# Kernel tuning notes

Hardware: AMD Instinct MI355X
Metric: run time of the kernel (lower is better)

The kernel has to match this reference:

```python
import jax, jax.numpy as jnp
import numpy as np

DIM = 512
NL = 4
P = 8
B = 4
L = 8192  # byte-level sequence length
LP = L // P  # patch-level sequence length


def _ln(x, g, b, eps=1e-5):
    m = jnp.mean(x, axis=-1, keepdims=True)
    v = jnp.mean((x - m) ** 2, axis=-1, keepdims=True)
    return (x - m) * jax.lax.rsqrt(v + eps) * g + b


def setup_inputs() -> dict:
    key = jax.random.key(0)
    ks = jax.random.split(key, 24)
    s = 0.02
    inp = {
        "bytes_in": jax.random.randint(ks[0], (B, L), 0, 256, dtype=jnp.int32),
        "byte_emb": jax.random.normal(ks[1], (256, DIM), jnp.float32) * s,
        # patch encoder Conv1d(kernel=stride=P): weight laid out [P, D_in, D_out]
        "enc_w": jax.random.normal(ks[2], (P, DIM, DIM), jnp.float32) * s,
        "enc_b": jnp.zeros((DIM,), jnp.float32),
        "hash_proj": jax.random.normal(ks[3], (DIM, DIM), jnp.float32) * s,
        # per-layer stacked params
        "qkv_w": jax.random.normal(ks[4], (NL, DIM, 3 * DIM), jnp.float32) * s,
        "qkv_b": jnp.zeros((NL, 3 * DIM), jnp.float32),
        "gate_w": jax.random.normal(ks[5], (NL, DIM, DIM), jnp.float32) * s,
        "gate_b": jnp.zeros((NL, DIM), jnp.float32),
        "ln1_g": jnp.ones((NL, DIM), jnp.float32),
        "ln1_b": jnp.zeros((NL, DIM), jnp.float32),
        "mlp_w1": jax.random.normal(ks[6], (NL, DIM, 4 * DIM), jnp.float32) * s,
        "mlp_b1": jnp.zeros((NL, 4 * DIM), jnp.float32),
        "mlp_w2": jax.random.normal(ks[7], (NL, 4 * DIM, DIM), jnp.float32) * s,
        "mlp_b2": jnp.zeros((NL, DIM), jnp.float32),
        "ln2_g": jnp.ones((NL, DIM), jnp.float32),
        "ln2_b": jnp.zeros((NL, DIM), jnp.float32),
        # patch decoder ConvTranspose1d(kernel=stride=P): weight [D_in, P, D_out]
        "dec_w": jax.random.normal(ks[8], (DIM, P, DIM), jnp.float32) * s,
        "dec_b": jnp.zeros((DIM,), jnp.float32),
        "head_w": jax.random.normal(ks[9], (DIM, 256), jnp.float32) * s,
        "head_b": jnp.zeros((256,), jnp.float32),
    }
    return inp


def reference(bytes_in, byte_emb, enc_w, enc_b, hash_proj,
              qkv_w, qkv_b, gate_w, gate_b, ln1_g, ln1_b,
              mlp_w1, mlp_b1, mlp_w2, mlp_b2, ln2_g, ln2_b,
              dec_w, dec_b, head_w, head_b):
    # byte embedding: [B, L, D]
    x = byte_emb[bytes_in]
    # non-overlapping Conv1d(kernel=stride=P) == patch-wise contraction
    xp = x.reshape(B, LP, P, DIM)
    x = jnp.einsum('blpd,pdo->blo', xp, enc_w) + enc_b  # [B, LP, D]
    # hash projection
    x = x + jnp.tanh(x @ hash_proj)
    for i in range(NL):
        # LinearLatentKernel
        h = _ln(x, ln1_g[i], ln1_b[i])
        qkv = h @ qkv_w[i] + qkv_b[i]
        q, k, v = jnp.split(qkv, 3, axis=-1)
        kv_state = jnp.cumsum(k * v, axis=1)
        g = jax.nn.sigmoid(h @ gate_w[i] + gate_b[i])
        x = x + q * kv_state * g
        # MLP
        h = _ln(x, ln2_g[i], ln2_b[i])
        h = jax.nn.gelu(h @ mlp_w1[i] + mlp_b1[i], approximate=False)
        x = x + h @ mlp_w2[i] + mlp_b2[i]
    # ConvTranspose1d(kernel=stride=P): each patch expands to P positions
    y = jnp.einsum('bld,dpo->blpo', x, dec_w).reshape(B, L, DIM) + dec_b
    logits = y @ head_w + head_b  # [B, L, 256]
    return logits
```

## Files before the change

kernel.cpp:

```cpp
#include <hip/hip_runtime.h>
#include <hip/hip_bf16.h>
#include <math.h>

#define DIMD 512
#define NLAYER 4
#define PP 8
#define BBATCH 4
#define LBYTES 8192
#define LPATCH 1024
#define MROWS (BBATCH * LPATCH)

#define NCHUNK 64
#define CLEN   16
#define QGS    (4 * DIMD)

typedef __bf16 bf16x8 __attribute__((ext_vector_type(8)));
typedef float f32x4 __attribute__((ext_vector_type(4)));
typedef unsigned short u16x4 __attribute__((ext_vector_type(4)));
typedef unsigned short u16x8 __attribute__((ext_vector_type(8)));

__device__ __forceinline__ unsigned short f2bf(float f) {
    union { float f; unsigned u; } v; v.f = f;
    unsigned r = v.u + 0x7FFFu + ((v.u >> 16) & 1u);
    return (unsigned short)(r >> 16);
}
__device__ __forceinline__ float bf2f(unsigned short u) {
    union { unsigned u; float f; } v; v.u = ((unsigned)u) << 16;
    return v.f;
}

__device__ __forceinline__ void glds16(const unsigned short* g, unsigned short* l) {
    __builtin_amdgcn_global_load_lds((__attribute__((address_space(1))) void*)g,
                                     (__attribute__((address_space(3))) void*)l,
                                     16, 0, 0);
}

template<int TM, int ACT, bool BIAS, bool RES, bool OBF>
__global__ __launch_bounds__(256)
void mfma_gemm(const unsigned short* __restrict__ A, int lda, long aZ,
               const unsigned short* __restrict__ Bt, int ldb, long bZ,
               const float* __restrict__ bias,
               const float* __restrict__ res, int ldr,
               void* __restrict__ Cv, int ldc, long cZ, int K)
{
    constexpr int M_REP = TM / 32;
    __shared__ unsigned short As[TM * 32];
    __shared__ unsigned short Bs[128 * 32];

    const int tid = threadIdx.x;
    const int w = tid >> 6, l = tid & 63;
    const int row0 = blockIdx.x * TM;
    const int col0 = blockIdx.y * 128;
    A  += (size_t)blockIdx.z * aZ;
    Bt += (size_t)blockIdx.z * bZ;
    unsigned short* Cb = (unsigned short*)Cv + (size_t)blockIdx.z * cZ;
    float*          Cf = (float*)Cv          + (size_t)blockIdx.z * cZ;

    const int cA = w * 64 + l;
    const unsigned short* gA0 = A + (size_t)(row0 + (cA >> 2)) * lda + (cA & 3) * 8;
    const unsigned short* gB0 = Bt + (size_t)(col0 + (cA >> 2)) * ldb + (cA & 3) * 8;
    const unsigned short* gB1 = Bt + (size_t)(col0 + 64 + (cA >> 2)) * ldb + (cA & 3) * 8;
    unsigned short* lA0 = &As[w * 512];
    unsigned short* lB0 = &Bs[w * 512];
    unsigned short* lB1 = &Bs[2048 + w * 512];
    const unsigned short* gA1 = nullptr;
    unsigned short* lA1 = nullptr;
    if constexpr (TM == 128) {
        gA1 = A + (size_t)(row0 + 64 + (cA >> 2)) * lda + (cA & 3) * 8;
        lA1 = &As[2048 + w * 512];
    }

    const int wr = (w >> 1) * (TM / 2);
    const int wc = (w & 1) * 64;
    const int lr = l & 15, lk = (l >> 4) * 8;
    const int aBase = (wr + lr) * 32 + lk;
    const int bBase = (wc + lr) * 32 + lk;

    f32x4 acc[M_REP][4] = {};

    for (int k0 = 0; k0 < K; k0 += 32) {
        glds16(gA0, lA0);  gA0 += 32;
        if constexpr (TM == 128) { glds16(gA1, lA1); gA1 += 32; }
        glds16(gB0, lB0);  gB0 += 32;
        glds16(gB1, lB1);  gB1 += 32;
        __syncthreads();
        bf16x8 af[M_REP], bfr[4];
        #pragma unroll
        for (int m = 0; m < M_REP; m++)
            af[m] = *reinterpret_cast<const bf16x8*>(&As[aBase + m * 512]);
        #pragma unroll
        for (int n = 0; n < 4; n++)
            bfr[n] = *reinterpret_cast<const bf16x8*>(&Bs[bBase + n * 512]);
        #pragma unroll
        for (int m = 0; m < M_REP; m++)
            #pragma unroll
            for (int n = 0; n < 4; n++)
                acc[m][n] = __builtin_amdgcn_mfma_f32_16x16x32_bf16(
                    af[m], bfr[n], acc[m][n], 0, 0, 0);
        __syncthreads();
    }

    const int r0 = row0 + wr + (l >> 4) * 4;
    const int c0 = col0 + wc + lr;
    float bv[4] = {0.f, 0.f, 0.f, 0.f};
    if (BIAS) {
        #pragma unroll
        for (int n = 0; n < 4; n++) bv[n] = bias[c0 + n * 16];
    }
    #pragma unroll
    for (int m = 0; m < M_REP; m++) {
        #pragma unroll
        for (int j = 0; j < 4; j++) {
            const int row = r0 + m * 16 + j;
            #pragma unroll
            for (int n = 0; n < 4; n++) {
                float v = acc[m][n][j];
                if (BIAS) v += bv[n];
                if (ACT == 1) v = tanhf(v);
                if (ACT == 2) v = 0.5f * v * (1.f + erff(v * 0.70710678118f));
                if (RES) v += res[(size_t)row * ldr + c0 + n * 16];
                if (OBF) Cb[(size_t)row * ldc + c0 + n * 16] = f2bf(v);
                else     Cf[(size_t)row * ldc + c0 + n * 16] = v;
            }
        }
    }
}

__device__ __forceinline__ void packT64(float* sm, const float* __restrict__ in,
                                        unsigned short* __restrict__ out,
                                        int K, int N, int bk, int bn)
{
    float (*t)[66] = (float(*)[66])sm;
    const int k0 = bk * 64, n0 = bn * 64;
    const int r = threadIdx.x >> 5;
    const int c2 = (threadIdx.x & 31) * 2;
    #pragma unroll
    for (int i = 0; i < 8; i++) {
        float2 v = *(const float2*)(in + (size_t)(k0 + r + i * 8) * N + n0 + c2);
        *(float2*)&t[r + i * 8][c2] = v;
    }
    __syncthreads();
    const int tx = threadIdx.x & 63, ty = threadIdx.x >> 6;
    #pragma unroll
    for (int i = 0; i < 16; i++)
        out[(size_t)(n0 + ty + i * 4) * K + k0 + tx] = f2bf(t[tx][ty + i * 4]);
}

__device__ __forceinline__ void cast_body(const float* __restrict__ in,
                                          unsigned short* __restrict__ out, int blk)
{
    const long i = ((long)blk * 256 + threadIdx.x) * 8;
    float4 a = *(const float4*)(in + i);
    float4 b = *(const float4*)(in + i + 4);
    u16x8 o;
    o[0] = f2bf(a.x); o[1] = f2bf(a.y); o[2] = f2bf(a.z); o[3] = f2bf(a.w);
    o[4] = f2bf(b.x); o[5] = f2bf(b.y); o[6] = f2bf(b.z); o[7] = f2bf(b.w);
    *reinterpret_cast<u16x8*>(out + i) = o;
}

__global__ __launch_bounds__(256)
void megapack(const float* __restrict__ qkv_w, const float* __restrict__ gate_w,
              const float* __restrict__ mlp_w1, const float* __restrict__ mlp_w2,
              const float* __restrict__ hash_proj, const float* __restrict__ head_w,
              const float* __restrict__ enc_w, const float* __restrict__ dec_w,
              const float* __restrict__ byte_emb,
              const float* __restrict__ qkv_b, const float* __restrict__ gate_b,
              const float* __restrict__ dec_b, const float* __restrict__ head_b,
              unsigned short* __restrict__ wcat, unsigned short* __restrict__ w1T,
              unsigned short* __restrict__ w2T, unsigned short* __restrict__ whashT,
              unsigned short* __restrict__ hwT, unsigned short* __restrict__ encT,
              unsigned short* __restrict__ decb, unsigned short* __restrict__ embB,
              float* __restrict__ cbias, float* __restrict__ fb)
{
    __shared__ float sm[64 * 66];
    int id = blockIdx.x;
    if (id < 768) {
        int z = id / 192, r = id % 192;
        packT64(sm, qkv_w + (size_t)z * 512 * 1536, wcat + (size_t)z * 2048 * 512,
                512, 1536, r % 8, r / 8);
    } else if (id < 1024) {
        id -= 768; int z = id / 64, r = id % 64;
        packT64(sm, gate_w + (size_t)z * 512 * 512,
                wcat + (size_t)z * 2048 * 512 + (size_t)1536 * 512,
                512, 512, r % 8, r / 8);
    } else if (id < 2048) {
        id -= 1024; int z = id / 256, r = id % 256;
        packT64(sm, mlp_w1 + (size_t)z * 512 * 2048, w1T + (size_t)z * 2048 * 512,
                512, 2048, r % 8, r / 8);
    } else if (id < 3072) {
        id -= 2048; int z = id / 256, r = id % 256;
        packT64(sm, mlp_w2 + (size_t)z * 2048 * 512, w2T + (size_t)z * 512 * 2048,
                2048, 512, r & 31, r >> 5);
    } else if (id < 3136) {
        id -= 3072;
        packT64(sm, hash_proj, whashT, 512, 512, id % 8, id / 8);
    } else if (id < 3168) {
        id -= 3136;
        packT64(sm, head_w, hwT, 512, 256, id % 8, id / 8);
    } else if (id < 3680) {
        id -= 3168; int z = id / 64, r = id % 64;
        packT64(sm, enc_w + (size_t)z * 512 * 512, encT + (size_t)z * 512 * 512,
                512, 512, r % 8, r / 8);
    } else if (id < 4704) {
        cast_body(dec_w, decb, id - 3680);
    } else if (id < 4768) {
        cast_body(byte_emb, embB, id - 4704);
    } else if (id < 4800) {
        id -= 4768;
        const int i = id >> 3;
        const int n = (id & 7) * 256 + threadIdx.x;
        cbias[i * 2048 + n] = (n < 1536) ? qkv_b[i * 1536 + n] : gate_b[i * 512 + n - 1536];
    } else {
        const int o = threadIdx.x;
        float s = head_b[o];
        for (int d = 0; d < DIMD; d++) s = fmaf(dec_b[d], head_w[d * 256 + o], s);
        #pragma unroll
        for (int p = 0; p < PP; p++) fb[p * 256 + o] = s;
    }
}

__global__ __launch_bounds__(256)
void ln_kernel(const float* __restrict__ x, const float* __restrict__ g,
               const float* __restrict__ b, unsigned short* __restrict__ h)
{
    const int row = blockIdx.x * 4 + (threadIdx.x >> 6);
    const int lane = threadIdx.x & 63;
    const float* xr = x + (long)row * DIMD;
    float4 v0 = *(const float4*)(xr + lane * 8);
    float4 v1 = *(const float4*)(xr + lane * 8 + 4);
    float xv[8] = {v0.x, v0.y, v0.z, v0.w, v1.x, v1.y, v1.z, v1.w};
    float s = 0.f, q = 0.f;
    #pragma unroll
    for (int j = 0; j < 8; j++) { s += xv[j]; q += xv[j] * xv[j]; }
    #pragma unroll
    for (int off = 1; off < 64; off <<= 1) {
        s += __shfl_xor(s, off);
        q += __shfl_xor(q, off);
    }
    const float mean = s * (1.f / DIMD);
    const float var  = q * (1.f / DIMD) - mean * mean;
    const float rstd = rsqrtf(var + 1e-5f);
    float4 g0 = *(const float4*)(g + lane * 8);
    float4 g1 = *(const float4*)(g + lane * 8 + 4);
    float4 b0 = *(const float4*)(b + lane * 8);
    float4 b1 = *(const float4*)(b + lane * 8 + 4);
    float gv[8] = {g0.x, g0.y, g0.z, g0.w, g1.x, g1.y, g1.z, g1.w};
    float bb[8] = {b0.x, b0.y, b0.z, b0.w, b1.x, b1.y, b1.z, b1.w};
    u16x8 o;
    #pragma unroll
    for (int j = 0; j < 8; j++) o[j] = f2bf((xv[j] - mean) * rstd * gv[j] + bb[j]);
    *reinterpret_cast<u16x8*>(h + (long)row * DIMD + lane * 8) = o;
}

__global__ __launch_bounds__(128)
void embed_kernel(const int* __restrict__ bytes, const float* __restrict__ E,
                  const float* __restrict__ enc_b, float* __restrict__ x0,
                  unsigned short* __restrict__ x0b)
{
    const int patch = blockIdx.x;
    __shared__ int by[PP];
    if (threadIdx.x < PP) by[threadIdx.x] = bytes[patch * PP + threadIdx.x];
    __syncthreads();
    const int o = threadIdx.x * 4;
    float4 acc = *(const float4*)(enc_b + o);
    #pragma unroll
    for (int p = 0; p < PP; p++) {
        float4 e = *(const float4*)(E + ((long)(p * 256 + by[p])) * DIMD + o);
        acc.x += e.x; acc.y += e.y; acc.z += e.z; acc.w += e.w;
    }
    *(float4*)(x0 + (long)patch * DIMD + o) = acc;
    u16x4 ob; ob[0] = f2bf(acc.x); ob[1] = f2bf(acc.y);
    ob[2] = f2bf(acc.z); ob[3] = f2bf(acc.w);
    *reinterpret_cast<u16x4*>(x0b + (long)patch * DIMD + o) = ob;
}

__global__ __launch_bounds__(256)
void scan_partial(const unsigned short* __restrict__ qg, float* __restrict__ S)
{
    const int b = blockIdx.x >> 6, c = blockIdx.x & 63, d2 = threadIdx.x * 2;
    const unsigned short* base = qg + (size_t)(b * LPATCH + c * CLEN) * QGS;
    float s0 = 0.f, s1 = 0.f;
    for (int l = 0; l < CLEN; l++) {
        ushort2 kk = *(const ushort2*)(base + l * QGS + DIMD + d2);
        ushort2 vv = *(const ushort2*)(base + l * QGS + 2 * DIMD + d2);
        s0 = fmaf(bf2f(kk.x), bf2f(vv.x), s0);
        s1 = fmaf(bf2f(kk.y), bf2f(vv.y), s1);
    }
    *(float2*)(S + (size_t)(b * NCHUNK + c) * DIMD + d2) = make_float2(s0, s1);
}

__global__ __launch_bounds__(512)
void scan_prefix(float* __restrict__ S)
{
    const int b = blockIdx.x, d = threadIdx.x;
    float run = 0.f;
    #pragma unroll 4
    for (int c = 0; c < NCHUNK; c++) {
        float v = S[(b * NCHUNK + c) * DIMD + d];
        S[(b * NCHUNK + c) * DIMD + d] = run;
        run += v;
    }
}

__global__ __launch_bounds__(512)
void scan_apply_ln(const unsigned short* __restrict__ qg,
                   const float* __restrict__ S, float* __restrict__ x,
                   const float* __restrict__ lg, const float* __restrict__ lb,
                   unsigned short* __restrict__ h)
{
    const int b = blockIdx.x >> 6, c = blockIdx.x & 63;
    const int w = threadIdx.x >> 6, lane = threadIdx.x & 63;
    const int d0 = lane * 8;

    float kv[8];
    {
        const float* Sp = S + (size_t)(b * NCHUNK + c) * DIMD + d0;
        float4 a = *(const float4*)Sp;
        float4 bq = *(const float4*)(Sp + 4);
        kv[0] = a.x; kv[1] = a.y; kv[2] = a.z; kv[3] = a.w;
        kv[4] = bq.x; kv[5] = bq.y; kv[6] = bq.z; kv[7] = bq.w;
    }
    const int row0 = b * LPATCH + c * CLEN;
    for (int l = 0; l < 2 * w; l++) {
        const unsigned short* qb = qg + (size_t)(row0 + l) * QGS;
        u16x8 kk = *reinterpret_cast<const u16x8*>(qb + DIMD + d0);
        u16x8 vv = *reinterpret_cast<const u16x8*>(qb + 2 * DIMD + d0);
        #pragma unroll
        for (int j = 0; j < 8; j++) kv[j] = fmaf(bf2f(kk[j]), bf2f(vv[j]), kv[j]);
    }

    float gv[8], bv[8];
    {
        float4 g0 = *(const float4*)(lg + d0);
        float4 g1 = *(const float4*)(lg + d0 + 4);
        float4 b0 = *(const float4*)(lb + d0);
        float4 b1 = *(const float4*)(lb + d0 + 4);
        gv[0] = g0.x; gv[1] = g0.y; gv[2] = g0.z; gv[3] = g0.w;
        gv[4] = g1.x; gv[5] = g1.y; gv[6] = g1.z; gv[7] = g1.w;
        bv[0] = b0.x; bv[1] = b0.y; bv[2] = b0.z; bv[3] = b0.w;
        bv[4] = b1.x; bv[5] = b1.y; bv[6] = b1.z; bv[7] = b1.w;
    }

    for (int l = 2 * w; l < 2 * w + 2; l++) {
        const unsigned short* qb = qg + (size_t)(row0 + l) * QGS;
        u16x8 qq = *reinterpret_cast<const u16x8*>(qb + d0);
        u16x8 kk = *reinterpret_cast<const u16x8*>(qb + DIMD + d0);
        u16x8 vv = *reinterpret_cast<const u16x8*>(qb + 2 * DIMD + d0);
        u16x8 gg = *reinterpret_cast<const u16x8*>(qb + 3 * DIMD + d0);
        float* xr = x + (size_t)(row0 + l) * DIMD + d0;
        float4 xv0 = *(const float4*)xr;
        float4 xv1 = *(const float4*)(xr + 4);
        float xold[8] = {xv0.x, xv0.y, xv0.z, xv0.w, xv1.x, xv1.y, xv1.z, xv1.w};
        float xn[8];
        float s = 0.f, qs = 0.f;
        #pragma unroll
        for (int j = 0; j < 8; j++) {
            kv[j] = fmaf(bf2f(kk[j]), bf2f(vv[j]), kv[j]);
            const float sg = 1.f / (1.f + expf(-bf2f(gg[j])));
            const float nv = xold[j] + bf2f(qq[j]) * kv[j] * sg;
            xn[j] = nv; s += nv; qs += nv * nv;
        }
        *(float4*)xr       = make_float4(xn[0], xn[1], xn[2], xn[3]);
        *(float4*)(xr + 4) = make_float4(xn[4], xn[5], xn[6], xn[7]);
        #pragma unroll
        for (int off = 1; off < 64; off <<= 1) {
            s += __shfl_xor(s, off);
            qs += __shfl_xor(qs, off);
        }
        const float mean = s * (1.f / DIMD);
        const float var  = qs * (1.f / DIMD) - mean * mean;
        const float rstd = rsqrtf(var + 1e-5f);
        u16x8 ho;
        #pragma unroll
        for (int j = 0; j < 8; j++) ho[j] = f2bf((xn[j] - mean) * rstd * gv[j] + bv[j]);
        *reinterpret_cast<u16x8*>(h + (size_t)(row0 + l) * DIMD + d0) = ho;
    }
}

extern "C" void kernel_launch(void* const* d_in, const int* in_sizes, int n_in,
                              void* d_out, int out_size, void* d_ws, size_t ws_size,
                              hipStream_t stream)
{
    (void)in_sizes; (void)n_in; (void)out_size; (void)ws_size;

    const int*   bytes_in  = (const int*)d_in[0];
    const float* byte_emb  = (const float*)d_in[1];
    const float* enc_w     = (const float*)d_in[2];
    const float* enc_b     = (const float*)d_in[3];
    const float* hash_proj = (const float*)d_in[4];
    const float* qkv_w     = (const float*)d_in[5];
    const float* qkv_b     = (const float*)d_in[6];
    const float* gate_w    = (const float*)d_in[7];
    const float* gate_b    = (const float*)d_in[8];
    const float* ln1_g     = (const float*)d_in[9];
    const float* ln1_b     = (const float*)d_in[10];
    const float* mlp_w1    = (const float*)d_in[11];
    const float* mlp_b1    = (const float*)d_in[12];
    const float* mlp_w2    = (const float*)d_in[13];
    const float* mlp_b2    = (const float*)d_in[14];
    const float* ln2_g     = (const float*)d_in[15];
    const float* ln2_b     = (const float*)d_in[16];
    const float* dec_w     = (const float*)d_in[17];
    const float* dec_b     = (const float*)d_in[18];
    const float* head_w    = (const float*)d_in[19];
    const float* head_b    = (const float*)d_in[20];
    float* out = (float*)d_out;

    char* ws = (char*)d_ws;
    size_t o = 0;
    auto alloc = [&](size_t bytes) { char* p = ws + o; o += (bytes + 255) & ~(size_t)255; return p; };
    unsigned short* wcat   = (unsigned short*)alloc((size_t)4 * 2048 * 512 * 2);
    unsigned short* w1T    = (unsigned short*)alloc((size_t)4 * 2048 * 512 * 2);
    unsigned short* w2T    = (unsigned short*)alloc((size_t)4 * 512 * 2048 * 2);
    unsigned short* whashT = (unsigned short*)alloc((size_t)512 * 512 * 2);
    unsigned short* wWfT   = (unsigned short*)alloc((size_t)2048 * 512 * 2);
    unsigned short* encT   = (unsigned short*)alloc((size_t)8 * 512 * 512 * 2);
    unsigned short* hwT    = (unsigned short*)alloc((size_t)256 * 512 * 2);
    unsigned short* decb   = (unsigned short*)alloc((size_t)512 * 8 * 512 * 2);
    unsigned short* embB   = (unsigned short*)alloc((size_t)256 * 512 * 2);
    float* cbias           = (float*)alloc((size_t)4 * 2048 * 4);
    float* fb              = (float*)alloc(2048 * 4);
    float* E               = (float*)alloc((size_t)8 * 256 * 512 * 4);
    float* x               = (float*)alloc((size_t)MROWS * DIMD * 4);
    float* x0              = (float*)alloc((size_t)MROWS * DIMD * 4);
    unsigned short* x0b    = (unsigned short*)alloc((size_t)MROWS * DIMD * 2);
    unsigned short* h      = (unsigned short*)alloc((size_t)MROWS * DIMD * 2);
    unsigned short* xb     = (unsigned short*)alloc((size_t)MROWS * DIMD * 2);
    float* S               = (float*)alloc((size_t)BBATCH * NCHUNK * DIMD * 4);
    unsigned short* qg     = (unsigned short*)alloc((size_t)MROWS * 2048 * 2);
    unsigned short* hid    = (unsigned short*)alloc((size_t)MROWS * 2048 * 2);

    megapack<<<dim3(4801), 256, 0, stream>>>(
        qkv_w, gate_w, mlp_w1, mlp_w2, hash_proj, head_w, enc_w, dec_w, byte_emb,
        qkv_b, gate_b, dec_b, head_b,
        wcat, w1T, w2T, whashT, hwT, encT, decb, embB, cbias, fb);

    mfma_gemm<64, 0, false, false, true><<<dim3(4, 4, 8), 256, 0, stream>>>(
        hwT, 512, 0L, decb, PP * 512, 512L,
        nullptr, nullptr, 0, wWfT, 512, (long)256 * 512, 512);

    mfma_gemm<64, 0, false, false, false><<<dim3(4, 4, 8), 256, 0, stream>>>(
        embB, 512, 0L, encT, 512, (long)512 * 512,
        nullptr, nullptr, 0, E, 512, (long)256 * 512, 512);

    embed_kernel<<<dim3(MROWS), dim3(128), 0, stream>>>(bytes_in, E, enc_b, x0, x0b);

    mfma_gemm<64, 1, false, true, false><<<dim3(MROWS / 64, 4, 1), 256, 0, stream>>>(
        x0b, DIMD, 0L, whashT, DIMD, 0L, nullptr, x0, DIMD, x, DIMD, 0L, DIMD);

    for (int i = 0; i < NLAYER; i++) {
        ln_kernel<<<dim3(MROWS / 4), 256, 0, stream>>>(x, ln1_g + i * DIMD, ln1_b + i * DIMD, h);
        mfma_gemm<128, 0, true, false, true><<<dim3(MROWS / 128, 16, 1), 256, 0, stream>>>(
            h, DIMD, 0L, wcat + (size_t)i * 2048 * 512, DIMD, 0L,
            cbias + (size_t)i * 2048, nullptr, 0, qg, 2048, 0L, DIMD);
        scan_partial<<<dim3(BBATCH * NCHUNK), 256, 0, stream>>>(qg, S);
        scan_prefix<<<dim3(BBATCH), dim3(512), 0, stream>>>(S);
        scan_apply_ln<<<dim3(BBATCH * NCHUNK), dim3(512), 0, stream>>>(
            qg, S, x, ln2_g + i * DIMD, ln2_b + i * DIMD, h);
        mfma_gemm<128, 2, true, false, true><<<dim3(MROWS / 128, 16, 1), 256, 0, stream>>>(
            h, DIMD, 0L, w1T + (size_t)i * 2048 * 512, DIMD, 0L,
            mlp_b1 + (size_t)i * 2048, nullptr, 0, hid, 2048, 0L, DIMD);
        if (i < NLAYER - 1) {
            mfma_gemm<64, 0, true, true, false><<<dim3(MROWS / 64, 4, 1), 256, 0, stream>>>(
                hid, 2048, 0L, w2T + (size_t)i * 512 * 2048, 2048, 0L,
                mlp_b2 + (size_t)i * DIMD, x, DIMD, x, DIMD, 0L, 2048);
        } else {
            mfma_gemm<64, 0, true, true, true><<<dim3(MROWS / 64, 4, 1), 256, 0, stream>>>(
                hid, 2048, 0L, w2T + (size_t)i * 512 * 2048, 2048, 0L,
                mlp_b2 + (size_t)i * DIMD, x, DIMD, xb, DIMD, 0L, 2048);
        }
    }

    mfma_gemm<128, 0, true, false, false><<<dim3(MROWS / 128, 16, 1), 256, 0, stream>>>(
        xb, DIMD, 0L, wWfT, DIMD, 0L, fb, nullptr, 0, out, 2048, 0L, DIMD);
}
```

Before: 485.3 us.

## Fuse chunk k*v partial sums into QKV GEMM epilogue via interleaved weight layout

Reorders the packed QKV+gate weight columns so that each 64-column tile holds q, k, v and gate for the same 16 feature dims. The GEMM epilogue can then compute per-16-row chunk sums of k*v and write them straight to S, replacing the separate scan_partial and scan_prefix kernels. scan_apply_ln now builds the chunk prefix itself by summing all earlier chunk partials, which is O(c) redundant loads per block, and reads q/k/v/g at the new interleaved offsets. The net effect is two fewer launches per layer and no extra pass over qg, at the cost of more epilogue work and redundant prefix reads.

New measurement: 512.3 us. 5.6% more time.

```diff
diff --git a/kernel.cpp b/kernel.cpp
--- a/kernel.cpp
+++ b/kernel.cpp
@@ -35,13 +35,14 @@
                                      16, 0, 0);
 }
 
-template<int TM, int ACT, bool BIAS, bool RES, bool OBF>
+template<int TM, int ACT, bool BIAS, bool RES, bool OBF, bool SCAN = false>
 __global__ __launch_bounds__(256)
 void mfma_gemm(const unsigned short* __restrict__ A, int lda, long aZ,
                const unsigned short* __restrict__ Bt, int ldb, long bZ,
                const float* __restrict__ bias,
                const float* __restrict__ res, int ldr,
-               void* __restrict__ Cv, int ldc, long cZ, int K)
+               void* __restrict__ Cv, int ldc, long cZ, int K,
+               float* __restrict__ Sout)
 {
     constexpr int M_REP = TM / 32;
     __shared__ unsigned short As[TM * 32];
@@ -123,12 +124,34 @@
                 else     Cf[(size_t)row * ldc + c0 + n * 16] = v;
             }
         }
-    }
+        if constexpr (SCAN) {
+            float s = 0.f;
+            #pragma unroll
+            for (int j = 0; j < 4; j++)
+                s += (acc[m][1][j] + bv[1]) * (acc[m][2][j] + bv[2]);
+            s += __shfl_xor(s, 16);
+            s += __shfl_xor(s, 32);
+            if (l < 16) {
+                const int grow = row0 + wr + m * 16;
+                const int sb = grow >> 10, sc = (grow & 1023) >> 4;
+                const int tg = (col0 + wc) >> 6;
+                Sout[(size_t)((sb << 6) + sc) * DIMD + tg * 16 + l] = s;
+            }
+        }
+    }
+}
+
+__device__ __forceinline__ int permcol(int n, int mode) {
+    if (mode == 0) return n;
+    int tau, d;
+    if (mode == 1) { tau = n >> 9; d = n & 511; }
+    else           { tau = 3;      d = n; }
+    return ((d >> 4) << 6) + (tau << 4) + (d & 15);
 }
 
 __device__ __forceinline__ void packT64(float* sm, const float* __restrict__ in,
                                         unsigned short* __restrict__ out,
-                                        int K, int N, int bk, int bn)
+                                        int K, int N, int bk, int bn, int mode)
 {
     float (*t)[66] = (float(*)[66])sm;
     const int k0 = bk * 64, n0 = bn * 64;
@@ -143,7 +166,7 @@
     const int tx = threadIdx.x & 63, ty = threadIdx.x >> 6;
     #pragma unroll
     for (int i = 0; i < 16; i++)
-        out[(size_t)(n0 + ty + i * 4) * K + k0 + tx] = f2bf(t[tx][ty + i * 4]);
+        out[(size_t)permcol(n0 + ty + i * 4, mode) * K + k0 + tx] = f2bf(t[tx][ty + i * 4]);
 }
 
 __device__ __forceinline__ void cast_body(const float* __restrict__ in,
@@ -177,30 +200,30 @@
     if (id < 768) {
         int z = id / 192, r = id % 192;
         packT64(sm, qkv_w + (size_t)z * 512 * 1536, wcat + (size_t)z * 2048 * 512,
-                512, 1536, r % 8, r / 8);
+                512, 1536, r % 8, r / 8, 1);
     } else if (id < 1024) {
         id -= 768; int z = id / 64, r = id % 64;
         packT64(sm, gate_w + (size_t)z * 512 * 512,
-                wcat + (size_t)z * 2048 * 512 + (size_t)1536 * 512,
-                512, 512, r % 8, r / 8);
+                wcat + (size_t)z * 2048 * 512,
+                512, 512, r % 8, r / 8, 2);
     } else if (id < 2048) {
         id -= 1024; int z = id / 256, r = id % 256;
         packT64(sm, mlp_w1 + (size_t)z * 512 * 2048, w1T + (size_t)z * 2048 * 512,
-                512, 2048, r % 8, r / 8);
+                512, 2048, r % 8, r / 8, 0);
     } else if (id < 3072) {
         id -= 2048; int z = id / 256, r = id % 256;
         packT64(sm, mlp_w2 + (size_t)z * 2048 * 512, w2T + (size_t)z * 512 * 2048,
-                2048, 512, r & 31, r >> 5);
+                2048, 512, r & 31, r >> 5, 0);
     } else if (id < 3136) {
         id -= 3072;
-        packT64(sm, hash_proj, whashT, 512, 512, id % 8, id / 8);
+        packT64(sm, hash_proj, whashT, 512, 512, id % 8, id / 8, 0);
     } else if (id < 3168) {
         id -= 3136;
-        packT64(sm, head_w, hwT, 512, 256, id % 8, id / 8);
+        packT64(sm, head_w, hwT, 512, 256, id % 8, id / 8, 0);
     } else if (id < 3680) {
         id -= 3168; int z = id / 64, r = id % 64;
         packT64(sm, enc_w + (size_t)z * 512 * 512, encT + (size_t)z * 512 * 512,
-                512, 512, r % 8, r / 8);
+                512, 512, r % 8, r / 8, 0);
     } else if (id < 4704) {
         cast_body(dec_w, decb, id - 3680);
     } else if (id < 4768) {
@@ -209,7 +232,10 @@
         id -= 4768;
         const int i = id >> 3;
         const int n = (id & 7) * 256 + threadIdx.x;
-        cbias[i * 2048 + n] = (n < 1536) ? qkv_b[i * 1536 + n] : gate_b[i * 512 + n - 1536];
+        const int t = n >> 6, tau = (n >> 4) & 3, r = n & 15;
+        const int d = t * 16 + r;
+        cbias[i * 2048 + n] = (tau < 3) ? qkv_b[i * 1536 + tau * 512 + d]
+                                        : gate_b[i * 512 + d];
     } else {
         const int o = threadIdx.x;
         float s = head_b[o];
@@ -274,34 +300,6 @@
     *reinterpret_cast<u16x4*>(x0b + (long)patch * DIMD + o) = ob;
 }
 
-__global__ __launch_bounds__(256)
-void scan_partial(const unsigned short* __restrict__ qg, float* __restrict__ S)
-{
-    const int b = blockIdx.x >> 6, c = blockIdx.x & 63, d2 = threadIdx.x * 2;
-    const unsigned short* base = qg + (size_t)(b * LPATCH + c * CLEN) * QGS;
-    float s0 = 0.f, s1 = 0.f;
-    for (int l = 0; l < CLEN; l++) {
-        ushort2 kk = *(const ushort2*)(base + l * QGS + DIMD + d2);
-        ushort2 vv = *(const ushort2*)(base + l * QGS + 2 * DIMD + d2);
-        s0 = fmaf(bf2f(kk.x), bf2f(vv.x), s0);
-        s1 = fmaf(bf2f(kk.y), bf2f(vv.y), s1);
-    }
-    *(float2*)(S + (size_t)(b * NCHUNK + c) * DIMD + d2) = make_float2(s0, s1);
-}
-
-__global__ __launch_bounds__(512)
-void scan_prefix(float* __restrict__ S)
-{
-    const int b = blockIdx.x, d = threadIdx.x;
-    float run = 0.f;
-    #pragma unroll 4
-    for (int c = 0; c < NCHUNK; c++) {
-        float v = S[(b * NCHUNK + c) * DIMD + d];
-        S[(b * NCHUNK + c) * DIMD + d] = run;
-        run += v;
-    }
-}
-
 __global__ __launch_bounds__(512)
 void scan_apply_ln(const unsigned short* __restrict__ qg,
                    const float* __restrict__ S, float* __restrict__ x,
@@ -311,20 +309,22 @@
     const int b = blockIdx.x >> 6, c = blockIdx.x & 63;
     const int w = threadIdx.x >> 6, lane = threadIdx.x & 63;
     const int d0 = lane * 8;
-
-    float kv[8];
-    {
-        const float* Sp = S + (size_t)(b * NCHUNK + c) * DIMD + d0;
-        float4 a = *(const float4*)Sp;
-        float4 bq = *(const float4*)(Sp + 4);
-        kv[0] = a.x; kv[1] = a.y; kv[2] = a.z; kv[3] = a.w;
-        kv[4] = bq.x; kv[5] = bq.y; kv[6] = bq.z; kv[7] = bq.w;
-    }
+    const int colq = ((d0 >> 4) << 6) + (d0 & 15);
+
+    float kv[8] = {0.f, 0.f, 0.f, 0.f, 0.f, 0.f, 0.f, 0.f};
+    const float* Sb = S + (size_t)b * NCHUNK * DIMD + d0;
+    for (int j = 0; j < c; j++) {
+        float4 a = *(const float4*)(Sb + (size_t)j * DIMD);
+        float4 bq = *(const float4*)(Sb + (size_t)j * DIMD + 4);
+        kv[0] += a.x; kv[1] += a.y; kv[2] += a.z; kv[3] += a.w;
+        kv[4] += bq.x; kv[5] += bq.y; kv[6] += bq.z; kv[7] += bq.w;
+    }
+
     const int row0 = b * LPATCH + c * CLEN;
     for (int l = 0; l < 2 * w; l++) {
-        const unsigned short* qb = qg + (size_t)(row0 + l) * QGS;
-        u16x8 kk = *reinterpret_cast<const u16x8*>(qb + DIMD + d0);
-        u16x8 vv = *reinterpret_cast<const u16x8*>(qb + 2 * DIMD + d0);
+        const unsigned short* qb = qg + (size_t)(row0 + l) * QGS + colq;
+        u16x8 kk = *reinterpret_cast<const u16x8*>(qb + 16);
+        u16x8 vv = *reinterpret_cast<const u16x8*>(qb + 32);
         #pragma unroll
         for (int j = 0; j < 8; j++) kv[j] = fmaf(bf2f(kk[j]), bf2f(vv[j]), kv[j]);
     }
@@ -342,11 +342,11 @@
     }
 
     for (int l = 2 * w; l < 2 * w + 2; l++) {
-        const unsigned short* qb = qg + (size_t)(row0 + l) * QGS;
-        u16x8 qq = *reinterpret_cast<const u16x8*>(qb + d0);
-        u16x8 kk = *reinterpret_cast<const u16x8*>(qb + DIMD + d0);
-        u16x8 vv = *reinterpret_cast<const u16x8*>(qb + 2 * DIMD + d0);
-        u16x8 gg = *reinterpret_cast<const u16x8*>(qb + 3 * DIMD + d0);
+        const unsigned short* qb = qg + (size_t)(row0 + l) * QGS + colq;
+        u16x8 qq = *reinterpret_cast<const u16x8*>(qb);
+        u16x8 kk = *reinterpret_cast<const u16x8*>(qb + 16);
+        u16x8 vv = *reinterpret_cast<const u16x8*>(qb + 32);
+        u16x8 gg = *reinterpret_cast<const u16x8*>(qb + 48);
         float* xr = x + (size_t)(row0 + l) * DIMD + d0;
         float4 xv0 = *(const float4*)xr;
         float4 xv1 = *(const float4*)(xr + 4);
@@ -437,40 +437,38 @@
 
     mfma_gemm<64, 0, false, false, true><<<dim3(4, 4, 8), 256, 0, stream>>>(
         hwT, 512, 0L, decb, PP * 512, 512L,
-        nullptr, nullptr, 0, wWfT, 512, (long)256 * 512, 512);
+        nullptr, nullptr, 0, wWfT, 512, (long)256 * 512, 512, nullptr);
 
     mfma_gemm<64, 0, false, false, false><<<dim3(4, 4, 8), 256, 0, stream>>>(
         embB, 512, 0L, encT, 512, (long)512 * 512,
-        nullptr, nullptr, 0, E, 512, (long)256 * 512, 512);
+        nullptr, nullptr, 0, E, 512, (long)256 * 512, 512, nullptr);
 
     embed_kernel<<<dim3(MROWS), dim3(128), 0, stream>>>(bytes_in, E, enc_b, x0, x0b);
 
     mfma_gemm<64, 1, false, true, false><<<dim3(MROWS / 64, 4, 1), 256, 0, stream>>>(
-        x0b, DIMD, 0L, whashT, DIMD, 0L, nullptr, x0, DIMD, x, DIMD, 0L, DIMD);
+        x0b, DIMD, 0L, whashT, DIMD, 0L, nullptr, x0, DIMD, x, DIMD, 0L, DIMD, nullptr);
 
     for (int i = 0; i < NLAYER; i++) {
         ln_kernel<<<dim3(MROWS / 4), 256, 0, stream>>>(x, ln1_g + i * DIMD, ln1_b + i * DIMD, h);
-        mfma_gemm<128, 0, true, false, true><<<dim3(MROWS / 128, 16, 1), 256, 0, stream>>>(
+        mfma_gemm<128, 0, true, false, true, true><<<dim3(MROWS / 128, 16, 1), 256, 0, stream>>>(
             h, DIMD, 0L, wcat + (size_t)i * 2048 * 512, DIMD, 0L,
-            cbias + (size_t)i * 2048, nullptr, 0, qg, 2048, 0L, DIMD);
-        scan_partial<<<dim3(BBATCH * NCHUNK), 256, 0, stream>>>(qg, S);
-        scan_prefix<<<dim3(BBATCH), dim3(512), 0, stream>>>(S);
+            cbias + (size_t)i * 2048, nullptr, 0, qg, 2048, 0L, DIMD, S);
         scan_apply_ln<<<dim3(BBATCH * NCHUNK), dim3(512), 0, stream>>>(
             qg, S, x, ln2_g + i * DIMD, ln2_b + i * DIMD, h);
         mfma_gemm<128, 2, true, false, true><<<dim3(MROWS / 128, 16, 1), 256, 0, stream>>>(
             h, DIMD, 0L, w1T + (size_t)i * 2048 * 512, DIMD, 0L,
-            mlp_b1 + (size_t)i * 2048, nullptr, 0, hid, 2048, 0L, DIMD);
+            mlp_b1 + (size_t)i * 2048, nullptr, 0, hid, 2048, 0L, DIMD, nullptr);
         if (i < NLAYER - 1) {
             mfma_gemm<64, 0, true, true, false><<<dim3(MROWS / 64, 4, 1), 256, 0, stream>>>(
                 hid, 2048, 0L, w2T + (size_t)i * 512 * 2048, 2048, 0L,
-                mlp_b2 + (size_t)i * DIMD, x, DIMD, x, DIMD, 0L, 2048);
+                mlp_b2 + (size_t)i * DIMD, x, DIMD, x, DIMD, 0L, 2048, nullptr);
         } else {
             mfma_gemm<64, 0, true, true, true><<<dim3(MROWS / 64, 4, 1), 256, 0, stream>>>(
                 hid, 2048, 0L, w2T + (size_t)i * 512 * 2048, 2048, 0L,
-                mlp_b2 + (size_t)i * DIMD, x, DIMD, xb, DIMD, 0L, 2048);
+                mlp_b2 + (size_t)i * DIMD, x, DIMD, xb, DIMD, 0L, 2048, nullptr);
         }
     }
 
     mfma_gemm<128, 0, true, false, false><<<dim3(MROWS / 128, 16, 1), 256, 0, stream>>>(
-        xb, DIMD, 0L, wWfT, DIMD, 0L, fb, nullptr, 0, out, 2048, 0L, DIMD);
-}
+        xb, DIMD, 0L, wWfT, DIMD, 0L, fb, nullptr, 0, out, 2048, 0L, DIMD, nullptr);
+}
```
